# Kernel tuning notes

Measured on AMD Instinct MI355X. Metric: run time of the kernel, lower is better.

Reference implementation:

```python
import jax, jax.numpy as jnp
import numpy as np

jax.config.update("jax_enable_x64", True)  # exact int64 fixed-point requantization

QMIN, QMAX = 0, 255  # 8-bit asymmetric activations


def _mul_m0_shift(acc, M0, shift):
    """gemmlowp-style fixed-point rescale: round((acc*M0)>>31) >> shift (rounding)."""
    prod = acc.astype(jnp.int64) * M0.astype(jnp.int64)
    nudge = jnp.where(prod >= 0, jnp.int64(1 << 30), jnp.int64(1 - (1 << 30)))
    hi = (prod + nudge) >> 31  # rounding-doubling high mul
    sh = shift.astype(jnp.int64)
    return (hi + (jnp.int64(1) << (sh - 1))) >> sh  # rounding right shift


def _requant(acc, M0, shift, z_out):
    return jnp.clip(_mul_m0_shift(acc, M0, shift) + z_out, QMIN, QMAX).astype(jnp.int32)


def _qconv(q, w, z_in, M0, shift, z_out, pad):
    # int8-style conv: subtract input zero-point, integer accumulate (exact in fp32
    # since |acc| < 2^24 by construction), then fixed-point requantize.
    xf = (q - z_in).astype(jnp.float32)
    acc = jax.lax.conv_general_dilated(
        xf, w, (1, 1), [(pad, pad), (pad, pad)],
        dimension_numbers=("NCHW", "OIHW", "NCHW"))
    return _requant(jnp.round(acc).astype(jnp.int64), M0, shift, z_out)


def _qbn(q, z_in, w, b, M0, shift, z_out):
    # fused quantized BN: per-channel integer affine + fixed-point requantize
    acc = (q.astype(jnp.int64) - z_in) * w.astype(jnp.int64)[None, :, None, None] \
          + b.astype(jnp.int64)[None, :, None, None]
    return _requant(acc, M0, shift, z_out)


def setup_inputs() -> dict:
    key = jax.random.key(0)
    ks = jax.random.split(key, 10)
    B, Cin, H, W = 32, 256, 56, 56
    width, Cout = 64, 256
    x = jax.random.randint(ks[0], (B, Cin, H, W), 0, 256, dtype=jnp.int32)
    w1 = jax.random.randint(ks[1], (width, Cin, 1, 1), -63, 64).astype(jnp.float32)
    w2 = jax.random.randint(ks[2], (width, width, 3, 3), -63, 64).astype(jnp.float32)
    w3 = jax.random.randint(ks[3], (Cout, width, 1, 1), -63, 64).astype(jnp.float32)
    bn1_w = jax.random.randint(ks[4], (width,), 100, 160).astype(jnp.float32)
    bn1_b = jax.random.randint(ks[5], (width,), -1000, 1000).astype(jnp.float32)
    bn2_w = jax.random.randint(ks[6], (width,), 100, 160).astype(jnp.float32)
    bn2_b = jax.random.randint(ks[7], (width,), -1000, 1000).astype(jnp.float32)
    bn3_w = jax.random.randint(ks[8], (Cout,), 100, 160).astype(jnp.float32)
    bn3_b = jax.random.randint(ks[9], (Cout,), -1000, 1000).astype(jnp.float32)
    conv_zin = jnp.array([128, 128, 128], jnp.int32)
    conv_m0 = jnp.array([1518500250] * 3, jnp.int32)
    conv_shift = jnp.array([9, 9, 9], jnp.int32)
    conv_zout = jnp.array([128, 128, 128], jnp.int32)
    bn_m0 = jnp.array([1073741824] * 3, jnp.int32)
    bn_shift = jnp.array([6, 6, 6], jnp.int32)
    bn_zout = jnp.array([128, 128, 128], jnp.int32)
    add_z = jnp.array([128, 128], jnp.int32)
    add_m0 = jnp.array([1073741824] * 2, jnp.int32)
    add_shift = jnp.array([1, 1], jnp.int32)
    add_zout = jnp.array(128, jnp.int32)
    return dict(x=x, w1=w1, w2=w2, w3=w3,
                bn1_w=bn1_w, bn1_b=bn1_b, bn2_w=bn2_w, bn2_b=bn2_b,
                bn3_w=bn3_w, bn3_b=bn3_b,
                conv_zin=conv_zin, conv_m0=conv_m0, conv_shift=conv_shift,
                conv_zout=conv_zout, bn_m0=bn_m0, bn_shift=bn_shift,
                bn_zout=bn_zout, add_z=add_z, add_m0=add_m0,
                add_shift=add_shift, add_zout=add_zout)


def reference(x, w1, w2, w3, bn1_w, bn1_b, bn2_w, bn2_b, bn3_w, bn3_b,
              conv_zin, conv_m0, conv_shift, conv_zout,
              bn_m0, bn_shift, bn_zout,
              add_z, add_m0, add_shift, add_zout):
    identity = x  # a_bit == target_bit -> rescale_matrix path skipped, conv_x = x
    out = _qconv(x, w1, conv_zin[0], conv_m0[0], conv_shift[0], conv_zout[0], 0)
    out = _qbn(out, conv_zout[0], bn1_w, bn1_b, bn_m0[0], bn_shift[0], bn_zout[0])
    out = _qconv(out, w2, conv_zin[1], conv_m0[1], conv_shift[1], conv_zout[1], 1)
    out = _qbn(out, conv_zout[1], bn2_w, bn2_b, bn_m0[1], bn_shift[1], bn_zout[1])
    out = _qconv(out, w3, conv_zin[2], conv_m0[2], conv_shift[2], conv_zout[2], 0)
    out = _qbn(out, conv_zout[2], bn3_w, bn3_b, bn_m0[2], bn_shift[2], bn_zout[2])
    # QuantizedAdd: rescale both branches to the output scale, add, clamp
    ra = _mul_m0_shift(identity.astype(jnp.int64) - add_z[0], add_m0[0], add_shift[0])
    rb = _mul_m0_shift(out.astype(jnp.int64) - add_z[1], add_m0[1], add_shift[1])
    return jnp.clip(ra + rb + add_zout, QMIN, QMAX).astype(jnp.int32)
```

## Files before the change

### kernel.cpp

```cpp
#include <hip/hip_runtime.h>


typedef int v4i __attribute__((ext_vector_type(4)));

#define BATCH 32
#define CIN 256
#define CMID 64
#define HW 3136
#define W56 56

#define WP_BYTES ((size_t)68 * 64 * 16)
#define WSUM_BYTES ((size_t)64 * 4)
#define T1_BYTES ((size_t)BATCH * HW * CMID)

__device__ __forceinline__ int rq_apply(int acc, int m0, long long cp, long long cn,
                                        int shm1, int zo) {
    long long prod = (long long)acc * m0;
    prod += (prod >= 0) ? cp : cn;
    int hi = (int)((unsigned long long)prod >> 32);
    int v = (hi >> shm1) + zo;
    return v < 0 ? 0 : (v > 255 ? 255 : v);
}

__device__ __forceinline__ int ms_apply(int xin, int m0, long long cp, long long cn,
                                        int shm1) {
    long long prod = (long long)xin * m0;
    prod += (prod >= 0) ? cp : cn;
    return ((int)((unsigned long long)prod >> 32)) >> shm1;
}

__device__ __forceinline__ unsigned int pk4x(int a0, int a1, int a2, int a3) {
    unsigned p01 = __builtin_amdgcn_perm((unsigned)a1, (unsigned)a0, 0x00000400u);
    unsigned p23 = __builtin_amdgcn_perm((unsigned)a3, (unsigned)a2, 0x04000000u);
    return __builtin_amdgcn_perm(p23, p01, 0x07060100u);
}

__device__ __forceinline__ v4i pack16f(const float* src, int stride) {
    v4i r;
#pragma unroll
    for (int d = 0; d < 4; ++d) {
        unsigned int u = 0;
#pragma unroll
        for (int by = 0; by < 4; ++by) {
            int v = (int)src[(d * 4 + by) * stride];
            u |= ((unsigned int)(v & 255)) << (8 * by);
        }
        r[d] = (int)u;
    }
    return r;
}

__global__ __launch_bounds__(256) void k_prep(
    const float* __restrict__ w1, const float* __restrict__ w2,
    const float* __restrict__ w3, v4i* __restrict__ wp, int* __restrict__ wsum)
{
    if (blockIdx.x < 17) {
        int id = blockIdx.x * 256 + threadIdx.x;
        int fid = id >> 6, lane = id & 63;
        int col = lane & 15, ci0 = (lane >> 4) * 16;
        const float* src;
        int stride;
        if (fid < 16) {
            int wv = fid >> 2, ks = fid & 3;
            src = w1 + (size_t)(wv * 16 + col) * 256 + ks * 64 + ci0;
            stride = 1;
        } else if (fid < 52) {
            int i = fid - 16, wv = i / 9, t = i - wv * 9;
            src = w2 + ((size_t)(wv * 16 + col) * 64 + ci0) * 9 + t;
            stride = 9;
        } else {
            int s = fid - 52;
            src = w3 + (size_t)(s * 16 + col) * 64 + ci0;
            stride = 1;
        }
        wp[fid * 64 + lane] = pack16f(src, stride);
    } else {
        int ch = threadIdx.x >> 2, t4 = threadIdx.x & 3;
        int s = 0;
        for (int i = 0; i < 64; ++i) s += (int)w1[(size_t)ch * 256 + t4 * 64 + i];
        s += __shfl_xor(s, 1);
        s += __shfl_xor(s, 2);
        if (t4 == 0) wsum[ch] = s;
    }
}

__global__ __launch_bounds__(256, 4) void k_conv1(
    const int* __restrict__ x, const v4i* __restrict__ wp1,
    const int* __restrict__ wsum1,
    const float* __restrict__ bn_w, const float* __restrict__ bn_b,
    const int* __restrict__ conv_zin, const int* __restrict__ conv_m0,
    const int* __restrict__ conv_shift, const int* __restrict__ conv_zout,
    const int* __restrict__ bn_m0, const int* __restrict__ bn_shift,
    const int* __restrict__ bn_zout, signed char* __restrict__ t1,
    unsigned char* __restrict__ xq)
{
    __shared__ v4i sm[560];
    const int tid = threadIdx.x, lane = tid & 63, wv = tid >> 6;
    const int col = lane & 15, koff = lane >> 4;
    const int b = blockIdx.y;
    const int hw0 = blockIdx.x * 112;
    const int co0 = wv * 16;

    v4i a[4];
#pragma unroll
    for (int ks = 0; ks < 4; ++ks) a[ks] = wp1[(wv * 4 + ks) * 64 + lane];

    const int cg = tid & 7, q = tid >> 3;
    const bool act = q < 28;
    const int* xbase = x + (size_t)b * CIN * HW + hw0 + 4 * q;
    unsigned char* xqb = xq + ((size_t)b * HW + hw0 + 4 * q) * 256 + cg * 8;

    v4i xa[8], xa2[8];
    if (act) {
#pragma unroll
        for (int j = 0; j < 8; ++j)
            xa[j] = *(const v4i*)(xbase + (size_t)(cg * 8 + j) * HW);
    }

    v4i acc[7];
#pragma unroll
    for (int i = 0; i < 7; ++i) acc[i] = (v4i){0, 0, 0, 0};

    unsigned long long* smu = (unsigned long long*)sm;
#pragma unroll
    for (int ks = 0; ks < 4; ++ks) {
        if (ks) __syncthreads();
        if (act) {
#pragma unroll
            for (int p = 0; p < 4; ++p) {
                unsigned lo = pk4x(xa[0][p], xa[1][p], xa[2][p], xa[3][p]) ^ 0x80808080u;
                unsigned hi = pk4x(xa[4][p], xa[5][p], xa[6][p], xa[7][p]) ^ 0x80808080u;
                unsigned long long pv = ((unsigned long long)hi << 32) | lo;
                smu[(q * 4 + p) * 10 + cg] = pv;
                *(unsigned long long*)(xqb + (size_t)p * 256 + ks * 64) = pv;
            }
        }
        __syncthreads();
        if (ks < 3 && act) {
#pragma unroll
            for (int j = 0; j < 8; ++j)
                xa2[j] = *(const v4i*)(xbase + (size_t)((ks + 1) * 64 + cg * 8 + j) * HW);
        }
#pragma unroll
        for (int nt = 0; nt < 7; ++nt) {
            v4i bf = sm[(nt * 16 + col) * 5 + koff];
            acc[nt] = __builtin_amdgcn_mfma_i32_16x16x64_i8(a[ks], bf, acc[nt], 0, 0, 0);
        }
        if (ks < 3) {
#pragma unroll
            for (int j = 0; j < 8; ++j) xa[j] = xa2[j];
        }
    }

    const int zin = conv_zin[0];
    const int corr0 = 128 - zin;
    const int cm0 = conv_m0[0], csh = conv_shift[0], czo = conv_zout[0];
    const int bm0 = bn_m0[0], bsh = bn_shift[0], bzo = bn_zout[0];
    const int zin2 = conv_zin[1];
    const long long cbv = 1LL << (30 + csh);
    const long long ccp = cbv + (1LL << 30), ccn = cbv + 1 - (1LL << 30);
    const int cshm1 = csh - 1;
    const long long bbv = 1LL << (30 + bsh);
    const long long bcp = bbv + (1LL << 30), bcn = bbv + 1 - (1LL << 30);
    const int bshm1 = bsh - 1;
    const int rowb = koff * 4;
    int bw[4], bbx[4], ws[4];
#pragma unroll
    for (int r = 0; r < 4; ++r) {
        bw[r] = (int)bn_w[co0 + rowb + r];
        bbx[r] = (int)bn_b[co0 + rowb + r] - czo * bw[r];
        ws[r] = wsum1[co0 + rowb + r];
    }
#pragma unroll
    for (int nt = 0; nt < 7; ++nt) {
        int n = b * HW + hw0 + nt * 16 + col;
        int e[4];
#pragma unroll
        for (int r = 0; r < 4; ++r) {
            int av = acc[nt][r] + corr0 * ws[r];
            int qv = rq_apply(av, cm0, ccp, ccn, cshm1, czo);
            int a2 = qv * bw[r] + bbx[r];
            int q2 = rq_apply(a2, bm0, bcp, bcn, bshm1, bzo);
            e[r] = q2 - zin2;
        }
        *(unsigned*)(t1 + (size_t)n * 64 + co0 + rowb) = pk4x(e[0], e[1], e[2], e[3]);
    }
}

__global__ __launch_bounds__(256, 4) void k_conv23(
    const signed char* __restrict__ t1, const v4i* __restrict__ wp2,
    const v4i* __restrict__ wp3,
    const float* __restrict__ bn2_w, const float* __restrict__ bn2_b,
    const float* __restrict__ bn3_w, const float* __restrict__ bn3_b,
    const unsigned char* __restrict__ xq,
    const int* __restrict__ conv_zin, const int* __restrict__ conv_m0,
    const int* __restrict__ conv_shift, const int* __restrict__ conv_zout,
    const int* __restrict__ bn_m0, const int* __restrict__ bn_shift,
    const int* __restrict__ bn_zout,
    const int* __restrict__ add_z, const int* __restrict__ add_m0,
    const int* __restrict__ add_shift, const int* __restrict__ add_zout,
    int* __restrict__ out)
{
    __shared__ v4i sm[840];
    __shared__ v4i t2s[320];
    const int tid = threadIdx.x, lane = tid & 63, wv = tid >> 6;
    const int col = lane & 15, koff = lane >> 4;
    const int b = blockIdx.y;
    const int r0 = blockIdx.x;
    const int co0 = wv * 16, rowb = koff * 4;

    v4i a[9];
#pragma unroll
    for (int t = 0; t < 9; ++t) a[t] = wp2[(wv * 9 + t) * 64 + lane];
    v4i a3x[4];
#pragma unroll
    for (int s = 0; s < 4; ++s) a3x[s] = wp3[(wv * 4 + s) * 64 + lane];

    const v4i* t1v = (const v4i*)t1;
#pragma unroll
    for (int k = 0; k < 3; ++k) {
        int idx = tid + k * 256;
        if (idx < 672) {
            int pixl = idx >> 2, part = idx & 3;
            int lrow = pixl / W56, gw = pixl - lrow * W56;
            int grow = r0 - 1 + lrow;
            v4i v = (v4i){0, 0, 0, 0};
            if ((unsigned)grow < 56u)
                v = t1v[((size_t)b * HW + grow * W56 + gw) * 4 + part];
            sm[pixl * 5 + part] = v;
        }
    }
    __syncthreads();

    v4i acc[4];
#pragma unroll
    for (int i = 0; i < 4; ++i) acc[i] = (v4i){0, 0, 0, 0};

#pragma unroll
    for (int kh = 0; kh < 3; ++kh) {
#pragma unroll
        for (int kw = 0; kw < 3; ++kw) {
            v4i af = a[kh * 3 + kw];
#pragma unroll
            for (int nt = 0; nt < 4; ++nt) {
                int sw = nt * 16 + col + kw - 1;
                bool valid = (unsigned)sw < 56u;
                v4i bf = sm[(kh * W56 + (valid ? sw : 0)) * 5 + koff];
                if (!valid) { bf[0] = 0; bf[1] = 0; bf[2] = 0; bf[3] = 0; }
                acc[nt] = __builtin_amdgcn_mfma_i32_16x16x64_i8(af, bf, acc[nt], 0, 0, 0);
            }
        }
    }

    int pxc[4];
#pragma unroll
    for (int nt = 0; nt < 4; ++nt) {
        int px = nt * 16 + col;
        pxc[nt] = px < 56 ? px : 55;
    }
    const unsigned char* xqb = xq + ((size_t)b * HW + r0 * W56) * 256 + wv * 64 + rowb;
    int xqv[4][4];
#pragma unroll
    for (int t = 0; t < 4; ++t)
#pragma unroll
        for (int nt = 0; nt < 4; ++nt)
            xqv[t][nt] = *(const int*)(xqb + (size_t)pxc[nt] * 256 + t * 16);

    {
        const int cm0 = conv_m0[1], csh = conv_shift[1], czo = conv_zout[1];
        const int bm0 = bn_m0[1], bsh = bn_shift[1], bzo = bn_zout[1];
        const int zin3 = conv_zin[2];
        const long long cbv = 1LL << (30 + csh);
        const long long ccp = cbv + (1LL << 30), ccn = cbv + 1 - (1LL << 30);
        const int cshm1 = csh - 1;
        const long long bbv = 1LL << (30 + bsh);
        const long long bcp = bbv + (1LL << 30), bcn = bbv + 1 - (1LL << 30);
        const int bshm1 = bsh - 1;
        int bw[4], bbx[4];
#pragma unroll
        for (int r = 0; r < 4; ++r) {
            bw[r] = (int)bn2_w[co0 + rowb + r];
            bbx[r] = (int)bn2_b[co0 + rowb + r] - czo * bw[r];
        }
#pragma unroll
        for (int nt = 0; nt < 4; ++nt) {
            int pix = nt * 16 + col;
            int e[4];
#pragma unroll
            for (int r = 0; r < 4; ++r) {
                int qv = rq_apply(acc[nt][r], cm0, ccp, ccn, cshm1, czo);
                int a2 = qv * bw[r] + bbx[r];
                int q2 = rq_apply(a2, bm0, bcp, bcn, bshm1, bzo);
                e[r] = q2 - zin3;
            }
            *(unsigned*)((char*)t2s + (size_t)(pix * 5 + wv) * 16 + koff * 4) =
                pk4x(e[0], e[1], e[2], e[3]);
        }
    }
    __syncthreads();

    const int cm0 = conv_m0[2], csh = conv_shift[2], czo = conv_zout[2];
    const int bm0 = bn_m0[2], bsh = bn_shift[2], bzo = bn_zout[2];
    const long long cb3 = 1LL << (30 + csh);
    const long long ccp = cb3 + (1LL << 30), ccn = cb3 + 1 - (1LL << 30);
    const int cshm1 = csh - 1;
    const long long bb3 = 1LL << (30 + bsh);
    const long long bcp = bb3 + (1LL << 30), bcn = bb3 + 1 - (1LL << 30);
    const int bshm1 = bsh - 1;
    const int az0 = add_z[0], az1 = add_z[1];
    const int corr = 128 - az0;
    const int am0 = add_m0[0], am1 = add_m0[1];
    const int ash0 = add_shift[0], ash1 = add_shift[1];
    const long long a0b = 1LL << (30 + ash0);
    const long long acp0 = a0b + (1LL << 30), acn0 = a0b + 1 - (1LL << 30);
    const int ashm0 = ash0 - 1;
    const long long a1b = 1LL << (30 + ash1);
    const long long acp1 = a1b + (1LL << 30), acn1 = a1b + 1 - (1LL << 30);
    const int ashm1 = ash1 - 1;
    const int azout = add_zout[0];

    int bw3[4][4], bbx3[4][4];
#pragma unroll
    for (int s = 0; s < 4; ++s)
#pragma unroll
        for (int r = 0; r < 4; ++r) {
            bw3[s][r] = (int)bn3_w[wv * 64 + s * 16 + rowb + r];
            bbx3[s][r] = (int)bn3_b[wv * 64 + s * 16 + rowb + r] - czo * bw3[s][r];
        }

    v4i bf[4];
#pragma unroll
    for (int nt = 0; nt < 4; ++nt) bf[nt] = t2s[(nt * 16 + col) * 5 + koff];

    int* ob = out + (size_t)b * CIN * HW + (size_t)r0 * W56;

#pragma unroll
    for (int t = 0; t < 4; ++t) {
        const int c0 = wv * 64 + t * 16;
        v4i acc3[4];
#pragma unroll
        for (int i = 0; i < 4; ++i) acc3[i] = (v4i){0, 0, 0, 0};
#pragma unroll
        for (int nt = 0; nt < 4; ++nt)
            acc3[nt] = __builtin_amdgcn_mfma_i32_16x16x64_i8(a3x[t], bf[nt], acc3[nt], 0, 0, 0);
#pragma unroll
        for (int nt = 0; nt < 4; ++nt) {
            int px = nt * 16 + col;
            bool st = px < 56;
#pragma unroll
            for (int r = 0; r < 4; ++r) {
                int sx = (int)(signed char)(((unsigned)xqv[t][nt]) >> (8 * r));
                int qv = rq_apply(acc3[nt][r], cm0, ccp, ccn, cshm1, czo);
                int a2 = qv * bw3[t][r] + bbx3[t][r];
                int q2 = rq_apply(a2, bm0, bcp, bcn, bshm1, bzo);
                int ra = ms_apply(sx + corr, am0, acp0, acn0, ashm0);
                int rb = ms_apply(q2 - az1, am1, acp1, acn1, ashm1);
                int res = ra + rb + azout;
                res = res < 0 ? 0 : (res > 255 ? 255 : res);
                if (st) ob[(size_t)(c0 + rowb + r) * HW + px] = res;
            }
        }
    }
}

extern "C" void kernel_launch(void* const* d_in, const int* in_sizes, int n_in,
                              void* d_out, int out_size, void* d_ws, size_t ws_size,
                              hipStream_t stream) {
    const int* x = (const int*)d_in[0];
    const float* w1 = (const float*)d_in[1];
    const float* w2 = (const float*)d_in[2];
    const float* w3 = (const float*)d_in[3];
    const float* bn1_w = (const float*)d_in[4];
    const float* bn1_b = (const float*)d_in[5];
    const float* bn2_w = (const float*)d_in[6];
    const float* bn2_b = (const float*)d_in[7];
    const float* bn3_w = (const float*)d_in[8];
    const float* bn3_b = (const float*)d_in[9];
    const int* conv_zin = (const int*)d_in[10];
    const int* conv_m0 = (const int*)d_in[11];
    const int* conv_shift = (const int*)d_in[12];
    const int* conv_zout = (const int*)d_in[13];
    const int* bn_m0 = (const int*)d_in[14];
    const int* bn_shift = (const int*)d_in[15];
    const int* bn_zout = (const int*)d_in[16];
    const int* add_z = (const int*)d_in[17];
    const int* add_m0 = (const int*)d_in[18];
    const int* add_shift = (const int*)d_in[19];
    const int* add_zout = (const int*)d_in[20];

    v4i* wp = (v4i*)d_ws;
    int* wsum1 = (int*)((char*)d_ws + WP_BYTES);
    signed char* t1 = (signed char*)d_ws + WP_BYTES + WSUM_BYTES;
    unsigned char* xq = (unsigned char*)t1 + T1_BYTES;

    const v4i* wp1 = wp;
    const v4i* wp2 = wp + 16 * 64;
    const v4i* wp3 = wp + 52 * 64;

    k_prep<<<dim3(18), dim3(256), 0, stream>>>(w1, w2, w3, wp, wsum1);
    k_conv1<<<dim3(28, 32), dim3(256), 0, stream>>>(x, wp1, wsum1, bn1_w, bn1_b,
        conv_zin, conv_m0, conv_shift, conv_zout, bn_m0, bn_shift, bn_zout, t1, xq);
    k_conv23<<<dim3(56, 32), dim3(256), 0, stream>>>(t1, wp2, wp3,
        bn2_w, bn2_b, bn3_w, bn3_b, xq,
        conv_zin, conv_m0, conv_shift, conv_zout, bn_m0, bn_shift, bn_zout,
        add_z, add_m0, add_shift, add_zout, (int*)d_out);
}
```

Measured before the change: 291.4 us.

## Split input packing into separate kernel and feed conv1 directly from packed bytes

Moves the int32-to-int8 NCHW-to-NHWC packing of x out of k_conv1 into a new k_pack kernel that transposes through LDS. k_conv1 then loads its MFMA B operands directly from the packed byte buffer in global memory, with no shared memory and no barriers. The aim is simpler, better-coalesced conv1 loads without LDS sync stalls. In exchange it adds a kernel launch and an extra read of the packed buffer from global memory, and it changes conv1's occupancy hint.

```diff
diff --git a/kernel.cpp b/kernel.cpp
--- a/kernel.cpp
+++ b/kernel.cpp
@@ -84,17 +84,48 @@
     }
 }
 
-__global__ __launch_bounds__(256, 4) void k_conv1(
-    const int* __restrict__ x, const v4i* __restrict__ wp1,
+__global__ __launch_bounds__(256) void k_pack(
+    const int* __restrict__ x, unsigned char* __restrict__ xq)
+{
+    __shared__ unsigned int lds[64 * 66];
+    const int tid = threadIdx.x;
+    const int b = blockIdx.y;
+    const int px0 = blockIdx.x * 64;
+    const int px = tid & 63, cb = (tid >> 6) * 64;
+    const int* xb = x + (size_t)b * CIN * HW + px0 + px;
+#pragma unroll
+    for (int i = 0; i < 16; ++i) {
+        int ch = cb + i * 4;
+        int v0 = xb[(size_t)(ch + 0) * HW];
+        int v1 = xb[(size_t)(ch + 1) * HW];
+        int v2 = xb[(size_t)(ch + 2) * HW];
+        int v3 = xb[(size_t)(ch + 3) * HW];
+        lds[px * 66 + (ch >> 2)] = pk4x(v0, v1, v2, v3) ^ 0x80808080u;
+    }
+    __syncthreads();
+    unsigned char* xqb = xq + ((size_t)b * HW + px0) * 256;
+#pragma unroll
+    for (int i = 0; i < 4; ++i) {
+        int flat = tid + i * 256;
+        int row = flat >> 4, off = (flat & 15) * 4;
+        v4i o;
+        o[0] = (int)lds[row * 66 + off + 0];
+        o[1] = (int)lds[row * 66 + off + 1];
+        o[2] = (int)lds[row * 66 + off + 2];
+        o[3] = (int)lds[row * 66 + off + 3];
+        *(v4i*)(xqb + (size_t)row * 256 + off * 4) = o;
+    }
+}
+
+__global__ __launch_bounds__(256, 2) void k_conv1(
+    const unsigned char* __restrict__ xq, const v4i* __restrict__ wp1,
     const int* __restrict__ wsum1,
     const float* __restrict__ bn_w, const float* __restrict__ bn_b,
     const int* __restrict__ conv_zin, const int* __restrict__ conv_m0,
     const int* __restrict__ conv_shift, const int* __restrict__ conv_zout,
     const int* __restrict__ bn_m0, const int* __restrict__ bn_shift,
-    const int* __restrict__ bn_zout, signed char* __restrict__ t1,
-    unsigned char* __restrict__ xq)
+    const int* __restrict__ bn_zout, signed char* __restrict__ t1)
 {
-    __shared__ v4i sm[560];
     const int tid = threadIdx.x, lane = tid & 63, wv = tid >> 6;
     const int col = lane & 15, koff = lane >> 4;
     const int b = blockIdx.y;
@@ -105,51 +136,21 @@
 #pragma unroll
     for (int ks = 0; ks < 4; ++ks) a[ks] = wp1[(wv * 4 + ks) * 64 + lane];
 
-    const int cg = tid & 7, q = tid >> 3;
-    const bool act = q < 28;
-    const int* xbase = x + (size_t)b * CIN * HW + hw0 + 4 * q;
-    unsigned char* xqb = xq + ((size_t)b * HW + hw0 + 4 * q) * 256 + cg * 8;
-
-    v4i xa[8], xa2[8];
-    if (act) {
-#pragma unroll
-        for (int j = 0; j < 8; ++j)
-            xa[j] = *(const v4i*)(xbase + (size_t)(cg * 8 + j) * HW);
-    }
+    const unsigned char* xqb = xq + ((size_t)b * HW + hw0) * 256 + koff * 16;
 
     v4i acc[7];
 #pragma unroll
     for (int i = 0; i < 7; ++i) acc[i] = (v4i){0, 0, 0, 0};
 
-    unsigned long long* smu = (unsigned long long*)sm;
 #pragma unroll
     for (int ks = 0; ks < 4; ++ks) {
-        if (ks) __syncthreads();
-        if (act) {
-#pragma unroll
-            for (int p = 0; p < 4; ++p) {
-                unsigned lo = pk4x(xa[0][p], xa[1][p], xa[2][p], xa[3][p]) ^ 0x80808080u;
-                unsigned hi = pk4x(xa[4][p], xa[5][p], xa[6][p], xa[7][p]) ^ 0x80808080u;
-                unsigned long long pv = ((unsigned long long)hi << 32) | lo;
-                smu[(q * 4 + p) * 10 + cg] = pv;
-                *(unsigned long long*)(xqb + (size_t)p * 256 + ks * 64) = pv;
-            }
-        }
-        __syncthreads();
-        if (ks < 3 && act) {
-#pragma unroll
-            for (int j = 0; j < 8; ++j)
-                xa2[j] = *(const v4i*)(xbase + (size_t)((ks + 1) * 64 + cg * 8 + j) * HW);
-        }
-#pragma unroll
-        for (int nt = 0; nt < 7; ++nt) {
-            v4i bf = sm[(nt * 16 + col) * 5 + koff];
-            acc[nt] = __builtin_amdgcn_mfma_i32_16x16x64_i8(a[ks], bf, acc[nt], 0, 0, 0);
-        }
-        if (ks < 3) {
-#pragma unroll
-            for (int j = 0; j < 8; ++j) xa[j] = xa2[j];
-        }
+        v4i bf[7];
+#pragma unroll
+        for (int nt = 0; nt < 7; ++nt)
+            bf[nt] = *(const v4i*)(xqb + (size_t)(nt * 16 + col) * 256 + ks * 64);
+#pragma unroll
+        for (int nt = 0; nt < 7; ++nt)
+            acc[nt] = __builtin_amdgcn_mfma_i32_16x16x64_i8(a[ks], bf[nt], acc[nt], 0, 0, 0);
     }
 
     const int zin = conv_zin[0];
@@ -398,8 +399,9 @@
     const v4i* wp3 = wp + 52 * 64;
 
     k_prep<<<dim3(18), dim3(256), 0, stream>>>(w1, w2, w3, wp, wsum1);
-    k_conv1<<<dim3(28, 32), dim3(256), 0, stream>>>(x, wp1, wsum1, bn1_w, bn1_b,
-        conv_zin, conv_m0, conv_shift, conv_zout, bn_m0, bn_shift, bn_zout, t1, xq);
+    k_pack<<<dim3(49, 32), dim3(256), 0, stream>>>(x, xq);
+    k_conv1<<<dim3(28, 32), dim3(256), 0, stream>>>(xq, wp1, wsum1, bn1_w, bn1_b,
+        conv_zin, conv_m0, conv_shift, conv_zout, bn_m0, bn_shift, bn_zout, t1);
     k_conv23<<<dim3(56, 32), dim3(256), 0, stream>>>(t1, wp2, wp3,
         bn2_w, bn2_b, bn3_w, bn3_b, xq,
         conv_zin, conv_m0, conv_shift, conv_zout, bn_m0, bn_shift, bn_zout,
```

Result: slower. 299.0 us (+2.6%).
